# Kernel optimization log

Measured on AMD Instinct MI355X. Metric: run time of the kernel, lower is better.

The kernel has to match this reference:

```python
import jax, jax.numpy as jnp
import numpy as np
from jax import lax

ALPHA = 4.0  # spikingjelly default Sigmoid surrogate alpha
EPS = 1e-5

@jax.custom_vjp
def spike_fn(u):
    return (u >= 0.0).astype(u.dtype)

def _spike_fwd(u):
    return spike_fn(u), u

def _spike_bwd(u, g):
    sg = jax.nn.sigmoid(ALPHA * u)
    return (g * ALPHA * sg * (1.0 - sg),)

spike_fn.defvjp(_spike_fwd, _spike_bwd)

def if_node(x):
    """Multi-step IF neuron (v_threshold=1, hard reset to 0) over leading T dim."""
    def step(v, xt):
        v = v + xt
        s = spike_fn(v - 1.0)
        v = v * (1.0 - s)
        return v, s
    _, spikes = lax.scan(step, jnp.zeros_like(x[0]), x)
    return spikes

def layer_norm(x, g, b):
    m = jnp.mean(x, axis=-1, keepdims=True)
    var = jnp.mean((x - m) ** 2, axis=-1, keepdims=True)
    return (x - m) * lax.rsqrt(var + EPS) * g + b

def setup_inputs() -> dict:
    key = jax.random.key(0)
    T, B, S, D = 4, 8, 1024, 768
    ks = jax.random.split(key, 5)
    scale = 1.0 / np.sqrt(D)
    inp = {
        "x": jax.random.normal(ks[0], (T, B, S, D), jnp.float32),
        "wq": jax.random.normal(ks[1], (D, D), jnp.float32) * scale,
        "wk": jax.random.normal(ks[2], (D, D), jnp.float32) * scale,
        "wv": jax.random.normal(ks[3], (D, D), jnp.float32) * scale,
        "wo": jax.random.normal(ks[4], (D, D), jnp.float32) * scale,
        "gq": jnp.ones((D,), jnp.float32), "bq": jnp.zeros((D,), jnp.float32),
        "gk": jnp.ones((D,), jnp.float32), "bk": jnp.zeros((D,), jnp.float32),
        "gv": jnp.ones((D,), jnp.float32), "bv": jnp.zeros((D,), jnp.float32),
        "go": jnp.ones((D,), jnp.float32), "bo": jnp.zeros((D,), jnp.float32),
    }
    return inp

def reference(x, wq, wk, wv, wo, gq, bq, gk, bk, gv, bv, go, bo):
    T, B, S, D = x.shape
    H, HD = 12, 64
    tmp = if_node(x)                                   # [T,B,S,D] spikes
    Q = if_node(layer_norm(tmp @ wq, gq, bq))
    K = if_node(layer_norm(tmp @ wk, gk, bk))
    V = if_node(layer_norm(tmp @ wv, gv, bv))
    # [T,B,S,H,HD] -> [T,B,H,S,HD]
    Q = Q.reshape(T, B, S, H, HD).transpose(0, 1, 3, 2, 4)
    K = K.reshape(T, B, S, H, HD).transpose(0, 1, 3, 2, 4)
    V = V.reshape(T, B, S, H, HD).transpose(0, 1, 3, 2, 4)
    QK = jnp.sum(Q * K, axis=-2, keepdims=True)        # [T,B,H,1,HD]
    QK = if_node(QK)                                   # talking_heads IF spikes
    QKV = V * QK                                       # broadcast over S
    QKV = QKV.transpose(0, 1, 3, 2, 4).reshape(T, B, S, D)
    return layer_norm(QKV @ wo, go, bo)
```

## Files before the change

### kernel.cpp

```cpp
#include <hip/hip_runtime.h>
#include <hip/hip_bf16.h>

#define T_ 4
#define B_ 8
#define S_ 1024
#define D_ 768
#define BS_ (B_*S_)
#define M_ (T_*B_*S_)
#define BSD_ (B_*S_*D_)
#define LN_EPS 1e-5f
#define TAU 4e-5f

typedef unsigned short u16;
typedef unsigned char u8;
typedef unsigned int u32;
typedef unsigned long long u64;
typedef __bf16 bf16x8 __attribute__((ext_vector_type(8)));
typedef float f32x4 __attribute__((ext_vector_type(4)));

__global__ __launch_bounds__(768)
void k_if_mask(const float* __restrict__ x, u64* __restrict__ Am, u16* __restrict__ Ab) {
    int bs = blockIdx.x;
    int d = threadIdx.x;
    int wv = d >> 6, lane = d & 63;
    float v = 0.f;
    for (int t = 0; t < T_; ++t) {
        v += x[(size_t)t * BSD_ + (size_t)bs * D_ + d];
        bool s = (v >= 1.0f);
        u64 m = __ballot(s);
        if (lane == 0) Am[((size_t)t * 12 + wv) * BS_ + bs] = m;
        Ab[(size_t)t * BSD_ + (size_t)bs * D_ + d] = s ? 0x3F80 : 0;
        if (s) v = 0.f;
    }
}

__global__ void k_wconv(const float* __restrict__ wq, const float* __restrict__ wk,
                        const float* __restrict__ wv, const float* __restrict__ wo,
                        u16* __restrict__ Whi, u16* __restrict__ Wlo, u16* __restrict__ Wo) {
    int idx = blockIdx.x * 256 + threadIdx.x;
    int mat = idx / (D_ * D_);
    int r = idx % (D_ * D_);
    int n = r / D_;
    int k = r % D_;
    const float* src = (mat == 0) ? wq : (mat == 1) ? wk : (mat == 2) ? wv : wo;
    float w = src[k * D_ + n];
    __bf16 hi = (__bf16)w;
    u16 uhi = __builtin_bit_cast(u16, hi);
    if (mat == 3) { Wo[r] = uhi; return; }
    float lo = w - (float)hi;
    u16 ulo = __builtin_bit_cast(u16, (__bf16)lo);
    Whi[(size_t)mat * D_ * D_ + r] = uhi;
    Wlo[(size_t)mat * D_ * D_ + r] = ulo;
}

__device__ __forceinline__ void gload16(const void* g, void* l) {
    __builtin_amdgcn_global_load_lds(
        (const __attribute__((address_space(1))) unsigned int*)g,
        (__attribute__((address_space(3))) unsigned int*)l, 16, 0, 0);
}

template<int NMATS>
__global__ __launch_bounds__(256)
void k_gemm(const u16* __restrict__ A,
            const u16* __restrict__ Bh0, const u16* __restrict__ Bl0, float* __restrict__ C0,
            const u16* __restrict__ Bh1, const u16* __restrict__ Bl1, float* __restrict__ C1,
            const u16* __restrict__ Bh2, const u16* __restrict__ Bl2, float* __restrict__ C2,
            int ntn, int N) {
    __shared__ __align__(16) u16 As[128 * 64];
    __shared__ __align__(16) u16 Bh[128 * 64];
    __shared__ __align__(16) u16 Bl[NMATS == 2 ? 128 * 64 : 8];
    int my = blockIdx.y;
    const u16* Bhi = (my == 0) ? Bh0 : (my == 1) ? Bh1 : Bh2;
    const u16* Blo = (my == 0) ? Bl0 : (my == 1) ? Bl1 : Bl2;
    float* C = (my == 0) ? C0 : (my == 1) ? C1 : C2;
    int bid = blockIdx.x;
    bid = (bid & 7) * (gridDim.x >> 3) + (bid >> 3);
    int bn = bid % ntn, bm = bid / ntn;
    int tid = threadIdx.x;
    int l = tid & 63, w = tid >> 6;
    int wr = w >> 1, wc = w & 1;
    int lan16 = l & 15, kh = l >> 4;

    f32x4 acc[4][4];
    #pragma unroll
    for (int m = 0; m < 4; ++m)
        #pragma unroll
        for (int n = 0; n < 4; ++n)
            #pragma unroll
            for (int r = 0; r < 4; ++r) acc[m][n][r] = 0.f;

    int srow[4], scol[4];
    #pragma unroll
    for (int j = 0; j < 4; ++j) {
        int li = j * 256 + tid;
        srow[j] = li >> 3;
        scol[j] = ((li & 7) ^ ((li >> 3) & 7)) * 8;
    }
    int wbase = (tid >> 6) << 10;

    int aoff[4][2], boff[4][2];
    #pragma unroll
    for (int m = 0; m < 4; ++m)
        #pragma unroll
        for (int s = 0; s < 2; ++s) {
            int Ra = wr * 64 + m * 16 + lan16;
            aoff[m][s] = Ra * 128 + (((s * 4 + kh) ^ (Ra & 7)) << 4);
            int Rb = wc * 64 + m * 16 + lan16;
            boff[m][s] = Rb * 128 + (((s * 4 + kh) ^ (Rb & 7)) << 4);
        }

    for (int kk = 0; kk < 768; kk += 64) {
        #pragma unroll
        for (int j = 0; j < 4; ++j) {
            gload16(A   + (size_t)(bm * 128 + srow[j]) * 768 + kk + scol[j],
                    (char*)As + j * 4096 + wbase);
            gload16(Bhi + (size_t)(bn * 128 + srow[j]) * 768 + kk + scol[j],
                    (char*)Bh + j * 4096 + wbase);
            if (NMATS == 2)
                gload16(Blo + (size_t)(bn * 128 + srow[j]) * 768 + kk + scol[j],
                        (char*)Bl + j * 4096 + wbase);
        }
        __syncthreads();
        #pragma unroll
        for (int s = 0; s < 2; ++s) {
            bf16x8 af[4], bh[4], bl[4];
            #pragma unroll
            for (int m = 0; m < 4; ++m)
                af[m] = *(const bf16x8*)((const char*)As + aoff[m][s]);
            #pragma unroll
            for (int n = 0; n < 4; ++n) {
                bh[n] = *(const bf16x8*)((const char*)Bh + boff[n][s]);
                if (NMATS == 2) bl[n] = *(const bf16x8*)((const char*)Bl + boff[n][s]);
            }
            #pragma unroll
            for (int m = 0; m < 4; ++m)
                #pragma unroll
                for (int n = 0; n < 4; ++n) {
                    acc[m][n] = __builtin_amdgcn_mfma_f32_16x16x32_bf16(af[m], bh[n], acc[m][n], 0, 0, 0);
                    if (NMATS == 2)
                        acc[m][n] = __builtin_amdgcn_mfma_f32_16x16x32_bf16(af[m], bl[n], acc[m][n], 0, 0, 0);
                }
        }
        __syncthreads();
    }
    #pragma unroll
    for (int m = 0; m < 4; ++m)
        #pragma unroll
        for (int n = 0; n < 4; ++n)
            #pragma unroll
            for (int r = 0; r < 4; ++r) {
                int crow = bm * 128 + wr * 64 + m * 16 + kh * 4 + r;
                int ccol = bn * 128 + wc * 64 + n * 16 + lan16;
                C[(size_t)crow * N + ccol] = acc[m][n][r];
            }
}

__global__ __launch_bounds__(256)
void k_lnif(const float* __restrict__ Y0, const float* __restrict__ Y1,
            const float* __restrict__ Y2,
            const float* __restrict__ gq, const float* __restrict__ bq,
            const float* __restrict__ gk, const float* __restrict__ bk,
            const float* __restrict__ gv, const float* __restrict__ bv,
            u8* __restrict__ Qs, u8* __restrict__ Ks, u8* __restrict__ Vs,
            int* __restrict__ rowlist, int* __restrict__ cnt, int mat0) {
    #pragma clang fp contract(off)
    int mat = mat0 + blockIdx.y;
    const float* Y = (mat == 0) ? Y0 : (mat == 1) ? Y1 : Y2;
    const float* g = (mat == 0) ? gq : (mat == 1) ? gk : gv;
    const float* bt = (mat == 0) ? bq : (mat == 1) ? bk : bv;
    u8* Sp = (mat == 0) ? Qs : (mat == 1) ? Ks : Vs;
    int row = blockIdx.x * 4 + (threadIdx.x >> 6);
    int lane = threadIdx.x & 63;
    float v[12];
    #pragma unroll
    for (int i = 0; i < 12; ++i) v[i] = 0.f;
    float gv_[12], bv_[12];
    #pragma unroll
    for (int i = 0; i < 12; ++i) { gv_[i] = g[lane + 64*i]; bv_[i] = bt[lane + 64*i]; }
    bool fl = false;
    for (int t = 0; t < T_; ++t) {
        size_t base = ((size_t)t * BS_ + row) * D_;
        float xv[12];
        double s = 0.0;
        #pragma unroll
        for (int i = 0; i < 12; ++i) { xv[i] = Y[base + lane + 64*i]; s += (double)xv[i]; }
        #pragma unroll
        for (int o = 1; o < 64; o <<= 1) s += __shfl_xor(s, o, 64);
        s = __shfl(s, 0, 64);
        float m = (float)(s / 768.0);
        float d[12];
        double q = 0.0;
        #pragma unroll
        for (int i = 0; i < 12; ++i) { d[i] = xv[i] - m; float sq = d[i]*d[i]; q += (double)sq; }
        #pragma unroll
        for (int o = 1; o < 64; o <<= 1) q += __shfl_xor(q, o, 64);
        q = __shfl(q, 0, 64);
        float var = (float)(q / 768.0);
        float inv = 1.0f / __fsqrt_rn(var + LN_EPS);
        #pragma unroll
        for (int i = 0; i < 12; ++i) {
            float yn = ((d[i] * inv) * gv_[i]) + bv_[i];
            v[i] += yn;
            fl = fl || (fabsf(v[i] - 1.0f) < TAU);
            bool sp = (v[i] >= 1.0f);
            Sp[base + lane + 64*i] = sp ? (u8)1 : (u8)0;
            if (sp) v[i] = 0.f;
        }
    }
    u64 bal = __ballot(fl);
    if (lane == 0 && bal != 0ull) {
        int slot = atomicAdd(cnt + mat, 1);
        rowlist[mat * BS_ + slot] = row;
    }
}

__global__ __launch_bounds__(768)
void k_repairT(const u64* __restrict__ Am,
               const float* __restrict__ wq, const float* __restrict__ wk,
               const float* __restrict__ wv,
               const float* __restrict__ gq, const float* __restrict__ bq,
               const float* __restrict__ gk, const float* __restrict__ bk,
               const float* __restrict__ gv, const float* __restrict__ bv,
               u8* __restrict__ Qs, u8* __restrict__ Ks, u8* __restrict__ Vs,
               const int* __restrict__ rowlist, const int* __restrict__ cnt) {
    #pragma clang fp contract(off)
    int mat = blockIdx.y;
    int nf = cnt[mat];
    const float* W = (mat == 0) ? wq : (mat == 1) ? wk : wv;
    const float* g = (mat == 0) ? gq : (mat == 1) ? gk : gv;
    const float* bb = (mat == 0) ? bq : (mat == 1) ? bk : bv;
    u8* Sp = (mat == 0) ? Qs : (mat == 1) ? Ks : Vs;
    const float4* Wv4 = (const float4*)W;

    __shared__ u64 mks[4][12];
    __shared__ int pops[4][12];
    __shared__ int cnt4[4];
    __shared__ u16 idxs[4][768];
    __shared__ float4 ys[4][192];
    __shared__ float2 mi_sh[4];
    __shared__ double redd[12];

    int tid = threadIdx.x;
    int t = tid / 192;
    int tg = tid % 192;

    for (int e = blockIdx.x; e < nf; e += gridDim.x) {
        int row = rowlist[mat * BS_ + e];

        if (tid < 48) {
            int tt = tid / 12, kw = tid % 12;
            u64 m = Am[((size_t)tt * 12 + kw) * BS_ + row];
            mks[tt][kw] = m;
            pops[tt][kw] = __popcll(m);
        }
        __syncthreads();
        if (tid < 48) {
            int tt = tid / 12, kw = tid % 12;
            int off = 0;
            for (int j = 0; j < kw; ++j) off += pops[tt][j];
            u64 m = mks[tt][kw];
            int kb0 = kw * 64;
            while (m) {
                int kb = __builtin_ctzll(m);
                m &= m - 1;
                idxs[tt][off++] = (u16)(kb0 + kb);
            }
            if (kw == 11) cnt4[tt] = off;
        }
        __syncthreads();

        int cn = cnt4[t];
        float y0 = 0.f, y1 = 0.f, y2 = 0.f, y3 = 0.f;
        const u16* il = idxs[t];
        #pragma unroll 8
        for (int i = 0; i < cn; ++i) {
            float4 w = Wv4[(size_t)il[i] * 192 + tg];
            y0 += w.x; y1 += w.y; y2 += w.z; y3 += w.w;
        }

        int lane = tid & 63;
        int wv_t = tg >> 6;
        double s = (double)y0 + (double)y1 + (double)y2 + (double)y3;
        #pragma unroll
        for (int o = 1; o < 64; o <<= 1) s += __shfl_xor(s, o, 64);
        if (lane == 0) redd[t * 3 + wv_t] = s;
        __syncthreads();
        double stot = redd[t * 3] + redd[t * 3 + 1] + redd[t * 3 + 2];
        float mean = (float)(stot / 768.0);
        float d0 = y0 - mean, d1 = y1 - mean, d2 = y2 - mean, d3 = y3 - mean;
        double q = (double)(d0*d0) + (double)(d1*d1) + (double)(d2*d2) + (double)(d3*d3);
        #pragma unroll
        for (int o = 1; o < 64; o <<= 1) q += __shfl_xor(q, o, 64);
        __syncthreads();
        if (lane == 0) redd[t * 3 + wv_t] = q;
        __syncthreads();
        double qtot = redd[t * 3] + redd[t * 3 + 1] + redd[t * 3 + 2];
        float var = (float)(qtot / 768.0);
        float inv = 1.0f / __fsqrt_rn(var + LN_EPS);

        ys[t][tg] = make_float4(y0, y1, y2, y3);
        if (tg == 0) mi_sh[t] = make_float2(mean, inv);
        __syncthreads();

        if (tid < 192) {
            float4 gd = ((const float4*)g)[tg];
            float4 bd = ((const float4*)bb)[tg];
            float4 yt[4];
            float2 mi[4];
            #pragma unroll
            for (int tt = 0; tt < 4; ++tt) { yt[tt] = ys[tt][tg]; mi[tt] = mi_sh[tt]; }
            uchar4 o4[4];
            #pragma unroll
            for (int j = 0; j < 4; ++j) {
                float gj = (j == 0) ? gd.x : (j == 1) ? gd.y : (j == 2) ? gd.z : gd.w;
                float bj = (j == 0) ? bd.x : (j == 1) ? bd.y : (j == 2) ? bd.z : bd.w;
                float v = 0.f;
                #pragma unroll
                for (int tt = 0; tt < 4; ++tt) {
                    float yj = (j == 0) ? yt[tt].x : (j == 1) ? yt[tt].y : (j == 2) ? yt[tt].z : yt[tt].w;
                    float d = yj - mi[tt].x;
                    float yn = ((d * mi[tt].y) * gj) + bj;
                    v += yn;
                    bool sp = (v >= 1.0f);
                    u8 sb = sp ? (u8)1 : (u8)0;
                    if (j == 0) o4[tt].x = sb;
                    if (j == 1) o4[tt].y = sb;
                    if (j == 2) o4[tt].z = sb;
                    if (j == 3) o4[tt].w = sb;
                    if (sp) v = 0.f;
                }
            }
            #pragma unroll
            for (int tt = 0; tt < 4; ++tt)
                *(uchar4*)(Sp + ((size_t)tt * BS_ + row) * D_ + tg * 4) = o4[tt];
        }
        __syncthreads();
    }
}

__global__ void k_qkred(const u8* __restrict__ Q, const u8* __restrict__ K,
                        float* __restrict__ QK) {
    int bid = blockIdx.x;
    int sg = bid & 31, tb = bid >> 5;
    int tid = threadIdx.x;
    int c4 = tid * 4;
    size_t base = (size_t)tb * S_ * D_ + (size_t)sg * 32 * D_;
    int acc[4] = {0, 0, 0, 0};
    for (int s = 0; s < 32; ++s) {
        uchar4 q = *(const uchar4*)(Q + base + (size_t)s * D_ + c4);
        uchar4 k = *(const uchar4*)(K + base + (size_t)s * D_ + c4);
        acc[0] += q.x & k.x; acc[1] += q.y & k.y; acc[2] += q.z & k.z; acc[3] += q.w & k.w;
    }
    float* dst = QK + (size_t)tb * D_ + c4;
    #pragma unroll
    for (int j = 0; j < 4; ++j) atomicAdd(dst + j, (float)acc[j]);
}

__global__ void k_qkif(const float* __restrict__ QK, u8* __restrict__ QKs) {
    int i = blockIdx.x * 256 + threadIdx.x;
    float v = 0.f;
    for (int t = 0; t < T_; ++t) {
        v += QK[t * (B_ * D_) + i];
        bool s = (v >= 1.0f);
        QKs[t * (B_ * D_) + i] = s ? 1 : 0;
        if (s) v = 0.f;
    }
}

__global__ void k_qkv(const u8* __restrict__ V, const u8* __restrict__ QKs,
                      u16* __restrict__ O) {
    size_t e = ((size_t)blockIdx.x * 256 + threadIdx.x) * 4;
    uchar4 v = *(const uchar4*)(V + e);
    size_t d = e % D_;
    size_t b = (e / ((size_t)S_ * D_)) % B_;
    size_t t = e / BSD_;
    uchar4 qk = *(const uchar4*)(QKs + t * (B_ * D_) + b * D_ + d);
    ushort4 o;
    o.x = (v.x & qk.x) ? 0x3F80 : 0;
    o.y = (v.y & qk.y) ? 0x3F80 : 0;
    o.z = (v.z & qk.z) ? 0x3F80 : 0;
    o.w = (v.w & qk.w) ? 0x3F80 : 0;
    *(ushort4*)(O + e) = o;
}

__device__ __forceinline__ float block_sum(float v, float* red) {
    #pragma unroll
    for (int o = 32; o > 0; o >>= 1) v += __shfl_down(v, o, 64);
    int lane = threadIdx.x & 63, w = threadIdx.x >> 6;
    __syncthreads();
    if (lane == 0) red[w] = v;
    __syncthreads();
    return (red[0] + red[1]) + (red[2] + red[3]);
}

__global__ __launch_bounds__(256)
void k_lnfinal(const float* __restrict__ Y, const float* __restrict__ g,
               const float* __restrict__ bt, float* __restrict__ out) {
    #pragma clang fp contract(off)
    __shared__ float red[4];
    size_t row = (size_t)blockIdx.x * D_;
    int tid = threadIdx.x;
    float y[3];
    float s = 0.f;
    #pragma unroll
    for (int j = 0; j < 3; ++j) { y[j] = Y[row + tid + j * 256]; s += y[j]; }
    float mean = block_sum(s, red) / 768.0f;
    float q = 0.f;
    #pragma unroll
    for (int j = 0; j < 3; ++j) { float d = y[j] - mean; q += d * d; }
    float var = block_sum(q, red) / 768.0f;
    float inv = 1.0f / __fsqrt_rn(var + LN_EPS);
    #pragma unroll
    for (int j = 0; j < 3; ++j) {
        int c = tid + j * 256;
        out[row + c] = (y[j] - mean) * inv * g[c] + bt[c];
    }
}

extern "C" void kernel_launch(void* const* d_in, const int* in_sizes, int n_in,
                              void* d_out, int out_size, void* d_ws, size_t ws_size,
                              hipStream_t stream) {
    const float* x  = (const float*)d_in[0];
    const float* wq = (const float*)d_in[1];
    const float* wk = (const float*)d_in[2];
    const float* wv = (const float*)d_in[3];
    const float* wo = (const float*)d_in[4];
    const float* gq = (const float*)d_in[5];
    const float* bq = (const float*)d_in[6];
    const float* gk = (const float*)d_in[7];
    const float* bk = (const float*)d_in[8];
    const float* gv = (const float*)d_in[9];
    const float* bv = (const float*)d_in[10];
    const float* go = (const float*)d_in[11];
    const float* bo = (const float*)d_in[12];
    float* out = (float*)d_out;

    char* ws = (char*)d_ws;
    size_t off = 0;
    auto alloc = [&](size_t bytes) -> void* {
        void* p = ws + off;
        off += (bytes + 255) & ~(size_t)255;
        return p;
    };
    u64* Am    = (u64*)alloc((size_t)T_ * 12 * BS_ * 8);
    u16* Ab    = (u16*)alloc((size_t)M_ * D_ * 2);
    float* Y0  = (float*)alloc((size_t)M_ * D_ * 4);
    u8* Qs     = (u8*)alloc((size_t)M_ * D_);
    u8* Ks     = (u8*)alloc((size_t)M_ * D_);
    u8* Vs     = (u8*)alloc((size_t)M_ * D_);
    u16* Whi   = (u16*)alloc((size_t)3 * D_ * D_ * 2);
    u16* Wlo   = (u16*)alloc((size_t)3 * D_ * D_ * 2);
    u16* Wo    = (u16*)alloc((size_t)D_ * D_ * 2);
    float* QK  = (float*)alloc((size_t)T_ * B_ * D_ * 4);
    u8* QKs    = (u8*)alloc((size_t)T_ * B_ * D_);
    int* rowlist = (int*)alloc((size_t)3 * BS_ * 4);
    int* cnt   = (int*)alloc(256);
    float* Y1  = (float*)alloc((size_t)M_ * D_ * 4);
    float* Y2  = (float*)alloc((size_t)M_ * D_ * 4);
    bool fused = (off <= ws_size);
    if (!fused) { Y1 = Y0; Y2 = Y0; }

    hipMemsetAsync(QK, 0, (size_t)T_ * B_ * D_ * 4, stream);
    hipMemsetAsync(cnt, 0, 12, stream);

    k_if_mask<<<BS_, 768, 0, stream>>>(x, Am, Ab);
    k_wconv<<<(4 * D_ * D_) / 256, 256, 0, stream>>>(wq, wk, wv, wo, Whi, Wlo, Wo);
    const int ntn = D_ / 128;
    const int gemm_grid = (M_ / 128) * ntn;
    const u16* WhiQ = Whi + 0 * D_ * D_; const u16* WloQ = Wlo + 0 * D_ * D_;
    const u16* WhiK = Whi + 1 * D_ * D_; const u16* WloK = Wlo + 1 * D_ * D_;
    const u16* WhiV = Whi + 2 * D_ * D_; const u16* WloV = Wlo + 2 * D_ * D_;
    if (fused) {
        k_gemm<2><<<dim3(gemm_grid, 3), 256, 0, stream>>>(Ab,
            WhiQ, WloQ, Y0, WhiK, WloK, Y1, WhiV, WloV, Y2, ntn, D_);
        k_lnif<<<dim3(BS_ / 4, 3), 256, 0, stream>>>(Y0, Y1, Y2,
            gq, bq, gk, bk, gv, bv, Qs, Ks, Vs, rowlist, cnt, 0);
    } else {
        k_gemm<2><<<dim3(gemm_grid, 1), 256, 0, stream>>>(Ab,
            WhiQ, WloQ, Y0, WhiQ, WloQ, Y0, WhiQ, WloQ, Y0, ntn, D_);
        k_lnif<<<dim3(BS_ / 4, 1), 256, 0, stream>>>(Y0, Y0, Y0,
            gq, bq, gk, bk, gv, bv, Qs, Ks, Vs, rowlist, cnt, 0);
        k_gemm<2><<<dim3(gemm_grid, 1), 256, 0, stream>>>(Ab,
            WhiK, WloK, Y0, WhiK, WloK, Y0, WhiK, WloK, Y0, ntn, D_);
        k_lnif<<<dim3(BS_ / 4, 1), 256, 0, stream>>>(Y0, Y0, Y0,
            gq, bq, gk, bk, gv, bv, Qs, Ks, Vs, rowlist, cnt, 1);
        k_gemm<2><<<dim3(gemm_grid, 1), 256, 0, stream>>>(Ab,
            WhiV, WloV, Y0, WhiV, WloV, Y0, WhiV, WloV, Y0, ntn, D_);
        k_lnif<<<dim3(BS_ / 4, 1), 256, 0, stream>>>(Y0, Y0, Y0,
            gq, bq, gk, bk, gv, bv, Qs, Ks, Vs, rowlist, cnt, 2);
    }
    k_repairT<<<dim3(1024, 3), 768, 0, stream>>>(Am, wq, wk, wv, gq, bq, gk, bk, gv, bv,
                                                 Qs, Ks, Vs, rowlist, cnt);
    k_qkred<<<T_ * B_ * 32, 192, 0, stream>>>(Qs, Ks, QK);
    k_qkif<<<(B_ * D_) / 256, 256, 0, stream>>>(QK, QKs);
    k_qkv<<<(M_ * D_) / 4 / 256, 256, 0, stream>>>(Vs, QKs, Ab);
    k_gemm<1><<<dim3(gemm_grid, 1), 256, 0, stream>>>(Ab,
        Wo, Wo, Y0, Wo, Wo, Y0, Wo, Wo, Y0, ntn, D_);
    k_lnfinal<<<M_, 256, 0, stream>>>(Y0, go, bo, out);
}
```

Baseline: 572.9 us.

## Add element-level repair stage before full-row fp32 repair

New measurement: 580.2 us. About the same (+1.3%).

```diff
diff --git a/kernel.cpp b/kernel.cpp
--- a/kernel.cpp
+++ b/kernel.cpp
@@ -10,6 +10,8 @@
 #define BSD_ (B_*S_*D_)
 #define LN_EPS 1e-5f
 #define TAU 4e-5f
+#define TAU2 8e-6f
+#define ECAP (1 << 20)
 
 typedef unsigned short u16;
 typedef unsigned char u8;
@@ -162,7 +164,8 @@
             const float* __restrict__ gk, const float* __restrict__ bk,
             const float* __restrict__ gv, const float* __restrict__ bv,
             u8* __restrict__ Qs, u8* __restrict__ Ks, u8* __restrict__ Vs,
-            int* __restrict__ rowlist, int* __restrict__ cnt, int mat0) {
+            float2* __restrict__ MI, u32* __restrict__ elist, int* __restrict__ ecnt,
+            int mat0) {
     #pragma clang fp contract(off)
     int mat = mat0 + blockIdx.y;
     const float* Y = (mat == 0) ? Y0 : (mat == 1) ? Y1 : Y2;
@@ -172,12 +175,12 @@
     int row = blockIdx.x * 4 + (threadIdx.x >> 6);
     int lane = threadIdx.x & 63;
     float v[12];
-    #pragma unroll
-    for (int i = 0; i < 12; ++i) v[i] = 0.f;
+    bool fl[12];
+    #pragma unroll
+    for (int i = 0; i < 12; ++i) { v[i] = 0.f; fl[i] = false; }
     float gv_[12], bv_[12];
     #pragma unroll
     for (int i = 0; i < 12; ++i) { gv_[i] = g[lane + 64*i]; bv_[i] = bt[lane + 64*i]; }
-    bool fl = false;
     for (int t = 0; t < T_; ++t) {
         size_t base = ((size_t)t * BS_ + row) * D_;
         float xv[12];
@@ -197,20 +200,87 @@
         q = __shfl(q, 0, 64);
         float var = (float)(q / 768.0);
         float inv = 1.0f / __fsqrt_rn(var + LN_EPS);
+        if (lane == 0) MI[((size_t)mat * 4 + t) * BS_ + row] = make_float2(m, inv);
         #pragma unroll
         for (int i = 0; i < 12; ++i) {
             float yn = ((d[i] * inv) * gv_[i]) + bv_[i];
             v[i] += yn;
-            fl = fl || (fabsf(v[i] - 1.0f) < TAU);
+            fl[i] = fl[i] || (fabsf(v[i] - 1.0f) < TAU);
             bool sp = (v[i] >= 1.0f);
             Sp[base + lane + 64*i] = sp ? (u8)1 : (u8)0;
             if (sp) v[i] = 0.f;
         }
     }
-    u64 bal = __ballot(fl);
-    if (lane == 0 && bal != 0ull) {
-        int slot = atomicAdd(cnt + mat, 1);
-        rowlist[mat * BS_ + slot] = row;
+    #pragma unroll
+    for (int i = 0; i < 12; ++i) {
+        if (fl[i]) {
+            int slot = atomicAdd(ecnt, 1);
+            if (slot < ECAP)
+                elist[slot] = ((u32)mat << 23) | ((u32)row << 10) | (u32)(lane + 64*i);
+        }
+    }
+}
+
+__global__ __launch_bounds__(256)
+void k_repair2(const u64* __restrict__ Am,
+               const float* __restrict__ wq, const float* __restrict__ wk,
+               const float* __restrict__ wv, const float2* __restrict__ MI,
+               const float* __restrict__ gq, const float* __restrict__ bq,
+               const float* __restrict__ gk, const float* __restrict__ bk,
+               const float* __restrict__ gv, const float* __restrict__ bv,
+               u8* __restrict__ Qs, u8* __restrict__ Ks, u8* __restrict__ Vs,
+               const u32* __restrict__ elist, const int* __restrict__ ecnt,
+               int* __restrict__ rowlist2, int* __restrict__ cnt2) {
+    #pragma clang fp contract(off)
+    int nf = *ecnt;
+    if (nf > ECAP) nf = ECAP;
+    int t = threadIdx.x & 3;
+    int gid = (blockIdx.x * 256 + threadIdx.x) >> 2;
+    int ngroups = (gridDim.x * 256) >> 2;
+    int lane = threadIdx.x & 63;
+    int gbase = lane & ~3;
+    for (int e = gid; e < nf; e += ngroups) {
+        u32 p = elist[e];
+        int mat = p >> 23;
+        int row = (p >> 10) & 0x1FFF;
+        int col = p & 0x3FF;
+        const float* W = (mat == 0) ? wq : (mat == 1) ? wk : wv;
+        const float* g = (mat == 0) ? gq : (mat == 1) ? gk : gv;
+        const float* bb = (mat == 0) ? bq : (mat == 1) ? bk : bv;
+        u8* Sp = (mat == 0) ? Qs : (mat == 1) ? Ks : Vs;
+        float y = 0.f;
+        for (int kw = 0; kw < 12; ++kw) {
+            u64 m = Am[((size_t)t * 12 + kw) * BS_ + row];
+            const float* wp = W + (size_t)(kw * 64) * D_ + col;
+            #pragma unroll 16
+            for (int kb = 0; kb < 64; ++kb) {
+                float w = wp[(size_t)kb * D_];
+                y += ((m >> kb) & 1ull) ? w : 0.0f;
+            }
+        }
+        float y0 = __shfl(y, gbase + 0, 64);
+        float y1 = __shfl(y, gbase + 1, 64);
+        float y2 = __shfl(y, gbase + 2, 64);
+        float y3 = __shfl(y, gbase + 3, 64);
+        float yt[4] = {y0, y1, y2, y3};
+        float gc = g[col], bc = bb[col];
+        float v = 0.f;
+        bool efl = false;
+        #pragma unroll
+        for (int tt = 0; tt < 4; ++tt) {
+            float2 mi = MI[((size_t)mat * 4 + tt) * BS_ + row];
+            float yn = (((yt[tt] - mi.x) * mi.y) * gc) + bc;
+            v += yn;
+            efl = efl || (fabsf(v - 1.0f) < TAU2);
+            bool sp = (v >= 1.0f);
+            if (tt == t)
+                Sp[((size_t)tt * BS_ + row) * D_ + col] = sp ? (u8)1 : (u8)0;
+            if (sp) v = 0.f;
+        }
+        if (efl && t == 0) {
+            int slot = atomicAdd(cnt2 + mat, 1);
+            rowlist2[mat * BS_ + slot] = row;
+        }
     }
 }
 
@@ -453,15 +523,19 @@
     u16* Wo    = (u16*)alloc((size_t)D_ * D_ * 2);
     float* QK  = (float*)alloc((size_t)T_ * B_ * D_ * 4);
     u8* QKs    = (u8*)alloc((size_t)T_ * B_ * D_);
-    int* rowlist = (int*)alloc((size_t)3 * BS_ * 4);
+    float2* MI = (float2*)alloc((size_t)3 * 4 * BS_ * 8);
+    u32* elist = (u32*)alloc((size_t)ECAP * 4);
+    int* rowlist2 = (int*)alloc((size_t)3 * BS_ * 4);
     int* cnt   = (int*)alloc(256);
     float* Y1  = (float*)alloc((size_t)M_ * D_ * 4);
     float* Y2  = (float*)alloc((size_t)M_ * D_ * 4);
     bool fused = (off <= ws_size);
     if (!fused) { Y1 = Y0; Y2 = Y0; }
+    int* cnt2 = cnt;
+    int* ecnt = cnt + 3;
 
     hipMemsetAsync(QK, 0, (size_t)T_ * B_ * D_ * 4, stream);
-    hipMemsetAsync(cnt, 0, 12, stream);
+    hipMemsetAsync(cnt, 0, 256, stream);
 
     k_if_mask<<<BS_, 768, 0, stream>>>(x, Am, Ab);
     k_wconv<<<(4 * D_ * D_) / 256, 256, 0, stream>>>(wq, wk, wv, wo, Whi, Wlo, Wo);
@@ -474,23 +548,25 @@
         k_gemm<2><<<dim3(gemm_grid, 3), 256, 0, stream>>>(Ab,
             WhiQ, WloQ, Y0, WhiK, WloK, Y1, WhiV, WloV, Y2, ntn, D_);
         k_lnif<<<dim3(BS_ / 4, 3), 256, 0, stream>>>(Y0, Y1, Y2,
-            gq, bq, gk, bk, gv, bv, Qs, Ks, Vs, rowlist, cnt, 0);
+            gq, bq, gk, bk, gv, bv, Qs, Ks, Vs, MI, elist, ecnt, 0);
     } else {
         k_gemm<2><<<dim3(gemm_grid, 1), 256, 0, stream>>>(Ab,
             WhiQ, WloQ, Y0, WhiQ, WloQ, Y0, WhiQ, WloQ, Y0, ntn, D_);
         k_lnif<<<dim3(BS_ / 4, 1), 256, 0, stream>>>(Y0, Y0, Y0,
-            gq, bq, gk, bk, gv, bv, Qs, Ks, Vs, rowlist, cnt, 0);
+            gq, bq, gk, bk, gv, bv, Qs, Ks, Vs, MI, elist, ecnt, 0);
         k_gemm<2><<<dim3(gemm_grid, 1), 256, 0, stream>>>(Ab,
             WhiK, WloK, Y0, WhiK, WloK, Y0, WhiK, WloK, Y0, ntn, D_);
         k_lnif<<<dim3(BS_ / 4, 1), 256, 0, stream>>>(Y0, Y0, Y0,
-            gq, bq, gk, bk, gv, bv, Qs, Ks, Vs, rowlist, cnt, 1);
+            gq, bq, gk, bk, gv, bv, Qs, Ks, Vs, MI, elist, ecnt, 1);
         k_gemm<2><<<dim3(gemm_grid, 1), 256, 0, stream>>>(Ab,
             WhiV, WloV, Y0, WhiV, WloV, Y0, WhiV, WloV, Y0, ntn, D_);
         k_lnif<<<dim3(BS_ / 4, 1), 256, 0, stream>>>(Y0, Y0, Y0,
-            gq, bq, gk, bk, gv, bv, Qs, Ks, Vs, rowlist, cnt, 2);
-    }
-    k_repairT<<<dim3(1024, 3), 768, 0, stream>>>(Am, wq, wk, wv, gq, bq, gk, bk, gv, bv,
-                                                 Qs, Ks, Vs, rowlist, cnt);
+            gq, bq, gk, bk, gv, bv, Qs, Ks, Vs, MI, elist, ecnt, 2);
+    }
+    k_repair2<<<256, 256, 0, stream>>>(Am, wq, wk, wv, MI, gq, bq, gk, bk, gv, bv,
+                                       Qs, Ks, Vs, elist, ecnt, rowlist2, cnt2);
+    k_repairT<<<dim3(512, 3), 768, 0, stream>>>(Am, wq, wk, wv, gq, bq, gk, bk, gv, bv,
+                                                Qs, Ks, Vs, rowlist2, cnt2);
     k_qkred<<<T_ * B_ * 32, 192, 0, stream>>>(Qs, Ks, QK);
     k_qkif<<<(B_ * D_) / 256, 256, 0, stream>>>(QK, QKs);
     k_qkv<<<(M_ * D_) / 4 / 256, 256, 0, stream>>>(Vs, QKs, Ab);
```
